# Optimization experiments

Measured on AMD Instinct MI355X. Metric: run time of the kernel, lower is better.

The kernel has to match this reference:

```python
import jax, jax.numpy as jnp
import numpy as np

CAR_DIM = 8
ESC_MAX_AGENT = 32
HID = 256
ACTION_DIM = 30
NUM_STATES = 64
BATCH = 8192
ENC_OUT = 1 + CAR_DIM * ESC_MAX_AGENT          # 257
Q_IN = 1 + CAR_DIM + CAR_DIM * ESC_MAX_AGENT   # 265


def setup_inputs() -> dict:
    key = jax.random.key(0)
    ks = jax.random.split(key, 9)
    s = jax.random.normal(ks[0], (BATCH, CAR_DIM + NUM_STATES * CAR_DIM), dtype=jnp.float32)
    def lin(k, fan_in, fan_out):
        bound = 1.0 / np.sqrt(fan_in)
        kw, kb = jax.random.split(k)
        W = jax.random.uniform(kw, (fan_in, fan_out), jnp.float32, -bound, bound)
        b = jax.random.uniform(kb, (fan_out,), jnp.float32, -bound, bound)
        return W, b
    W1, b1 = lin(ks[1], CAR_DIM, HID)
    W2, b2 = lin(ks[2], HID, ENC_OUT)
    Qw1, Qb1 = lin(ks[3], Q_IN, HID)
    Qw2, Qb2 = lin(ks[4], HID, ACTION_DIM)
    return {"s": s, "W1": W1, "b1": b1, "W2": W2, "b2": b2,
            "Qw1": Qw1, "Qb1": Qb1, "Qw2": Qw2, "Qb2": Qb2}


def reference(s, W1, b1, W2, b2, Qw1, Qb1, Qw2, Qb2):
    B = s.shape[0]
    self_states = s[:, :CAR_DIM]                                   # [B, C]
    surr = s[:, CAR_DIM:].reshape(B, -1, CAR_DIM)                  # [B, N, C]
    # sentinel agents: any coordinate exactly == -1 is skipped
    valid = ~jnp.any(surr == -1.0, axis=-1)                        # [B, N] bool
    h = jax.nn.relu(jnp.einsum('bnc,ch->bnh', surr, W1) + b1)      # [B, N, HID]
    enc = jax.nn.relu(jnp.einsum('bnh,he->bne', h, W2) + b2)       # [B, N, ENC_OUT]
    sum_outputs = jnp.sum(enc * valid[:, :, None].astype(enc.dtype), axis=1)  # [B, ENC_OUT]
    x = jnp.concatenate([self_states, sum_outputs], axis=1)        # [B, Q_IN]
    q = jax.nn.relu(x @ Qw1 + Qb1) @ Qw2 + Qb2                     # [B, ACTION_DIM]
    return q
```

## Files before the change

kernel.cpp:

```cpp
#include <hip/hip_runtime.h>

#define CAR 8
#define SROW 520
#define HID 256
#define EOUT 257
#define XPAD 288
#define ADIM 30

typedef __attribute__((ext_vector_type(8))) short sh8;
typedef __attribute__((ext_vector_type(4))) float f32x4;

__device__ __forceinline__ short f2bf(float f) {
  unsigned u = __builtin_bit_cast(unsigned, f);
  u += 0x7fffu + ((u >> 16) & 1u);
  return (short)(u >> 16);
}
__device__ __forceinline__ unsigned f2bf2(float a, float b) {
  unsigned ua = __builtin_bit_cast(unsigned, a);
  ua += 0x7fffu + ((ua >> 16) & 1u);
  unsigned ub = __builtin_bit_cast(unsigned, b);
  ub += 0x7fffu + ((ub >> 16) & 1u);
  return __builtin_amdgcn_perm(ub, ua, 0x07060302);
}
__device__ __forceinline__ unsigned pkt(float a, float b) {
  return __builtin_amdgcn_perm(__builtin_bit_cast(unsigned, b),
                               __builtin_bit_cast(unsigned, a), 0x07060302);
}

__global__ void k_prep(const float* __restrict__ W1, const float* __restrict__ b1,
                       const float* __restrict__ W2,
                       const float* __restrict__ Qw1, const float* __restrict__ Qw2,
                       short* __restrict__ w1f, short* __restrict__ w2f,
                       short* __restrict__ w3f, short* __restrict__ wq2f) {
  int idx = blockIdx.x * 256 + threadIdx.x;
  if (idx < 8192) {
    int mt = idx >> 9, r = idx & 511, lane = r >> 3, j = r & 7;
    int quad = lane >> 4, m = lane & 15;
    int hid = mt * 16 + m;
    float v = (quad == 0) ? W1[j * HID + hid]
            : (quad == 1 && j == 0) ? b1[hid] : 0.0f;
    w1f[idx] = f2bf(v);
    return;
  }
  int i2 = idx - 8192;
  if (i2 < 69632) {
    int ks = i2 / 8704, r = i2 % 8704;
    int nt = r >> 9, r2 = r & 511, lane = r2 >> 3, j = r2 & 7;
    int quad = lane >> 4, m = lane & 15;
    int k = ks * 32 + quad * 8 + j, n = nt * 16 + m;
    float v = (n < EOUT) ? W2[k * EOUT + n] : 0.0f;
    w2f[i2] = f2bf(v);
    return;
  }
  int i3 = i2 - 69632;
  if (i3 < 73728) {
    int ks = i3 >> 13, r = i3 & 8191;
    int nt = r >> 9, r2 = r & 511, lane = r2 >> 3, j = r2 & 7;
    int quad = lane >> 4, m = lane & 15;
    int k = ks * 32 + quad * 8 + j, n = nt * 16 + m;
    float v = (k < 265) ? Qw1[k * HID + n] : 0.0f;
    w3f[i3] = f2bf(v);
    return;
  }
  int i4 = i3 - 73728;
  if (i4 < 8192) {
    int ks = i4 >> 10, r = i4 & 1023;
    int nt = r >> 9, r2 = r & 511, lane = r2 >> 3, j = r2 & 7;
    int quad = lane >> 4, m = lane & 15;
    int k = ks * 32 + quad * 8 + j, n = nt * 16 + m;
    float v = (n < ADIM) ? Qw2[k * ADIM + n] : 0.0f;
    wq2f[i4] = f2bf(v);
  }
}

__global__ __launch_bounds__(256, 2)
void k_enc(const float* __restrict__ s, const short* __restrict__ w1f,
           const short* __restrict__ w2f, const float* __restrict__ b2,
           float* __restrict__ so288, int B) {
  __shared__ __align__(16) short hlds[2][16384];
  __shared__ float ninvp[4];

  const int tid = threadIdx.x;
  const int w = tid >> 6, lane = tid & 63;
  const int q = lane >> 4, m = lane & 15;
  const int be = w >> 1, half = w & 1;
  const size_t b0 = 2 * (size_t)blockIdx.x;
  int bg = (int)b0 + be; if (bg >= B) bg = B - 1;

  const float* srow0 = s + (size_t)bg * SROW + CAR;
  int4 pk = {0, 0, 0, 0};
  bool inv = false;
  if (lane < 32) {
    const float* sr = srow0 + (half * 32 + lane) * CAR;
    float4 f0 = ((const float4*)sr)[0], f1 = ((const float4*)sr)[1];
    inv = (f0.x == -1.f) | (f0.y == -1.f) | (f0.z == -1.f) | (f0.w == -1.f) |
          (f1.x == -1.f) | (f1.y == -1.f) | (f1.z == -1.f) | (f1.w == -1.f);
    if (!inv) {
      pk.x = (int)f2bf2(f0.x, f0.y); pk.y = (int)f2bf2(f0.z, f0.w);
      pk.z = (int)f2bf2(f1.x, f1.y); pk.w = (int)f2bf2(f1.z, f1.w);
    }
  }
  const float vflag = inv ? 0.f : 1.f;
  unsigned long long bal = __ballot(inv);
  if (lane == 0) ninvp[w] = (float)__popcll(bal);

  int4 p0, p1;
  p0.x = __shfl(pk.x, m, 64);      p0.y = __shfl(pk.y, m, 64);
  p0.z = __shfl(pk.z, m, 64);      p0.w = __shfl(pk.w, m, 64);
  p1.x = __shfl(pk.x, 16 + m, 64); p1.y = __shfl(pk.y, 16 + m, 64);
  p1.z = __shfl(pk.z, 16 + m, 64); p1.w = __shfl(pk.w, 16 + m, 64);
  const float vv0 = __shfl(vflag, m, 64);
  const float vv1 = __shfl(vflag, 16 + m, 64);
  if (q == 1) {
    p0.x = (vv0 != 0.f) ? 0x3f80 : 0; p0.y = p0.z = p0.w = 0;
    p1.x = (vv1 != 0.f) ? 0x3f80 : 0; p1.y = p1.z = p1.w = 0;
  } else if (q >= 2) {
    p0.x = p0.y = p0.z = p0.w = 0;   p1.x = p1.y = p1.z = p1.w = 0;
  }
  sh8 bs0 = __builtin_bit_cast(sh8, p0);
  sh8 bs1 = __builtin_bit_cast(sh8, p1);

  const int T0 = half * 2, T1 = half * 2 + 1;
#pragma unroll
  for (int mt = 0; mt < 16; ++mt) {
    sh8 af = *(const sh8*)(w1f + (mt * 64 + lane) * 8);
    f32x4 z = {0.f, 0.f, 0.f, 0.f};
    f32x4 c0 = __builtin_amdgcn_mfma_f32_16x16x32_bf16(af, bs0, z, 0, 0, 0);
    f32x4 c1 = __builtin_amdgcn_mfma_f32_16x16x32_bf16(af, bs1, z, 0, 0, 0);
    const int hidb = mt * 16 + q * 4;
    const int ks = hidb >> 5, qB = (hidb >> 3) & 3, js = hidb & 7;
    uint2 k0, k1;
    k0.x = pkt(fmaxf(c0[0], 0.f), fmaxf(c0[1], 0.f));
    k0.y = pkt(fmaxf(c0[2], 0.f), fmaxf(c0[3], 0.f));
    k1.x = pkt(fmaxf(c1[0], 0.f), fmaxf(c1[1], 0.f));
    k1.y = pkt(fmaxf(c1[2], 0.f), fmaxf(c1[3], 0.f));
    *(uint2*)(&hlds[be][((T0 * 8 + ks) * 64 + qB * 16 + m) * 8 + js]) = k0;
    *(uint2*)(&hlds[be][((T1 * 8 + ks) * 64 + qB * 16 + m) * 8 + js]) = k1;
  }
  __syncthreads();

  f32x4 acc[4][5][2];
#pragma unroll
  for (int mt = 0; mt < 4; ++mt)
#pragma unroll
    for (int i = 0; i < 5; ++i)
#pragma unroll
      for (int e = 0; e < 2; ++e) {
        f32x4 z = {0.f, 0.f, 0.f, 0.f};
        acc[mt][i][e] = z;
      }

  if (w == 0) {
    sh8 Bf[5];
#pragma unroll
    for (int i = 0; i < 5; ++i) {
      const int t = (i < 4) ? i : 16;
      Bf[i] = *(const sh8*)(w2f + ((0 * 17 + t) * 64 + lane) * 8);
    }
#pragma unroll
    for (int ks = 0; ks < 8; ++ks) {
      sh8 Bn[5];
      if (ks < 7) {
#pragma unroll
        for (int i = 0; i < 5; ++i) {
          const int t = (i < 4) ? i : 16;
          Bn[i] = *(const sh8*)(w2f + (((ks + 1) * 17 + t) * 64 + lane) * 8);
        }
      }
#pragma unroll
      for (int e = 0; e < 2; ++e) {
        sh8 A[4];
#pragma unroll
        for (int mt = 0; mt < 4; ++mt)
          A[mt] = *(const sh8*)(&hlds[e][((mt * 8 + ks) * 64 + lane) * 8]);
#pragma unroll
        for (int i = 0; i < 5; ++i)
#pragma unroll
          for (int mt = 0; mt < 4; ++mt)
            acc[mt][i][e] = __builtin_amdgcn_mfma_f32_16x16x32_bf16(A[mt], Bf[i], acc[mt][i][e], 0, 0, 0);
      }
      if (ks < 7) {
#pragma unroll
        for (int i = 0; i < 5; ++i) Bf[i] = Bn[i];
      }
    }
  } else {
    const int t0 = 4 * w;
    sh8 Bf[4];
#pragma unroll
    for (int i = 0; i < 4; ++i)
      Bf[i] = *(const sh8*)(w2f + ((0 * 17 + t0 + i) * 64 + lane) * 8);
#pragma unroll
    for (int ks = 0; ks < 8; ++ks) {
      sh8 Bn[4];
      if (ks < 7) {
#pragma unroll
        for (int i = 0; i < 4; ++i)
          Bn[i] = *(const sh8*)(w2f + (((ks + 1) * 17 + t0 + i) * 64 + lane) * 8);
      }
#pragma unroll
      for (int e = 0; e < 2; ++e) {
        sh8 A[4];
#pragma unroll
        for (int mt = 0; mt < 4; ++mt)
          A[mt] = *(const sh8*)(&hlds[e][((mt * 8 + ks) * 64 + lane) * 8]);
#pragma unroll
        for (int i = 0; i < 4; ++i)
#pragma unroll
          for (int mt = 0; mt < 4; ++mt)
            acc[mt][i][e] = __builtin_amdgcn_mfma_f32_16x16x32_bf16(A[mt], Bf[i], acc[mt][i][e], 0, 0, 0);
      }
      if (ks < 7) {
#pragma unroll
        for (int i = 0; i < 4; ++i) Bf[i] = Bn[i];
      }
    }
  }

  const float ninv[2] = {ninvp[0] + ninvp[1], ninvp[2] + ninvp[3]};
#pragma unroll
  for (int i = 0; i < 5; ++i) {
    if (i == 4 && w != 0) continue;
    const int t = (i < 4) ? 4 * w + i : 16;
    const int col = t * 16 + m;
    const float b2c = (col < EOUT) ? b2[col] : 0.f;
    const float rb2 = fmaxf(b2c, 0.f);
#pragma unroll
    for (int e = 0; e < 2; ++e) {
      float ssum = 0.f;
#pragma unroll
      for (int mt = 0; mt < 4; ++mt)
#pragma unroll
        for (int r = 0; r < 4; ++r)
          ssum += fmaxf(acc[mt][i][e][r] + b2c, 0.f);
      ssum += __shfl_xor(ssum, 16, 64);
      ssum += __shfl_xor(ssum, 32, 64);
      ssum -= ninv[e] * rb2;
      if (q == 0)
        so288[(b0 + e) * XPAD + CAR + col] = ssum;
    }
  }
  if (w == 1 || w == 2) {
    size_t rr = b0 + (w - 1); if (rr >= (size_t)B) rr = B - 1;
    if (lane < CAR)       so288[rr * XPAD + lane] = s[rr * SROW + lane];
    else if (lane < 16)   so288[rr * XPAD + 280 + (lane - 8)] = 0.f;
  }
}

__global__ __launch_bounds__(256, 2)
void k_q(const float* __restrict__ so288, const short* __restrict__ w3f,
         const float* __restrict__ Qb1, const short* __restrict__ wq2f,
         const float* __restrict__ Qb2, float* __restrict__ out, int B) {
  __shared__ __align__(16) short xf[2 * 9 * 64 * 8];
  __shared__ __align__(16) float H[32 * 260];
  const int tid = threadIdx.x;
  const int w = tid >> 6, lane = tid & 63;
  const int q = lane >> 4, m = lane & 15;
  const int b0 = blockIdx.x * 32;

#pragma unroll
  for (int it = 0; it < 5; ++it) {
    int sidx = tid + it * 256;
    if (sidx < 1152) {
      int mt = sidx / 576, rem = sidx % 576;
      int ks = rem >> 6, l = rem & 63;
      int lq = l >> 4, lm = l & 15;
      int row = b0 + mt * 16 + lm; if (row >= B) row = B - 1;
      const float* xp = so288 + (size_t)row * XPAD + ks * 32 + lq * 8;
      float4 xa = ((const float4*)xp)[0], xb = ((const float4*)xp)[1];
      int4 t = {(int)f2bf2(xa.x, xa.y), (int)f2bf2(xa.z, xa.w),
                (int)f2bf2(xb.x, xb.y), (int)f2bf2(xb.z, xb.w)};
      *(int4*)(xf + sidx * 8) = t;
    }
  }
  __syncthreads();

  f32x4 acc1[2][4];
#pragma unroll
  for (int mt = 0; mt < 2; ++mt)
#pragma unroll
    for (int i = 0; i < 4; ++i) {
      f32x4 z = {0.f, 0.f, 0.f, 0.f};
      acc1[mt][i] = z;
    }
#pragma unroll
  for (int ks = 0; ks < 9; ++ks) {
    sh8 A0 = *(const sh8*)(xf + ((0 * 9 + ks) * 64 + lane) * 8);
    sh8 A1 = *(const sh8*)(xf + ((1 * 9 + ks) * 64 + lane) * 8);
#pragma unroll
    for (int i = 0; i < 4; ++i) {
      sh8 Bf = *(const sh8*)(w3f + ((ks * 16 + 4 * w + i) * 64 + lane) * 8);
      acc1[0][i] = __builtin_amdgcn_mfma_f32_16x16x32_bf16(A0, Bf, acc1[0][i], 0, 0, 0);
      acc1[1][i] = __builtin_amdgcn_mfma_f32_16x16x32_bf16(A1, Bf, acc1[1][i], 0, 0, 0);
    }
  }
#pragma unroll
  for (int i = 0; i < 4; ++i) {
    const int hcol = (4 * w + i) * 16 + m;
    const float bq = Qb1[hcol];
#pragma unroll
    for (int mt = 0; mt < 2; ++mt)
#pragma unroll
      for (int r = 0; r < 4; ++r)
        H[(mt * 16 + q * 4 + r) * 260 + hcol] = fmaxf(acc1[mt][i][r] + bq, 0.f);
  }
  __syncthreads();

  const int mt2 = w >> 1, nt2 = w & 1;
  f32x4 acc2 = {0.f, 0.f, 0.f, 0.f};
#pragma unroll
  for (int ks = 0; ks < 8; ++ks) {
    const float* hp = H + (mt2 * 16 + m) * 260 + ks * 32 + q * 8;
    float4 ha = ((const float4*)hp)[0], hb = ((const float4*)hp)[1];
    int4 t = {(int)f2bf2(ha.x, ha.y), (int)f2bf2(ha.z, ha.w),
              (int)f2bf2(hb.x, hb.y), (int)f2bf2(hb.z, hb.w)};
    sh8 A2 = __builtin_bit_cast(sh8, t);
    sh8 Bf = *(const sh8*)(wq2f + ((ks * 2 + nt2) * 64 + lane) * 8);
    acc2 = __builtin_amdgcn_mfma_f32_16x16x32_bf16(A2, Bf, acc2, 0, 0, 0);
  }
  const int act = nt2 * 16 + m;
  if (act < ADIM) {
    const float bq = Qb2[act];
#pragma unroll
    for (int r = 0; r < 4; ++r) {
      const int row = b0 + mt2 * 16 + q * 4 + r;
      if (row < B) out[(size_t)row * ADIM + act] = acc2[r] + bq;
    }
  }
}

extern "C" void kernel_launch(void* const* d_in, const int* in_sizes, int n_in,
                              void* d_out, int out_size, void* d_ws, size_t ws_size,
                              hipStream_t stream) {
  const float* s   = (const float*)d_in[0];
  const float* W1  = (const float*)d_in[1];
  const float* b1  = (const float*)d_in[2];
  const float* W2  = (const float*)d_in[3];
  const float* b2  = (const float*)d_in[4];
  const float* Qw1 = (const float*)d_in[5];
  const float* Qb1 = (const float*)d_in[6];
  const float* Qw2 = (const float*)d_in[7];
  const float* Qb2 = (const float*)d_in[8];
  float* out = (float*)d_out;
  const int B = in_sizes[0] / SROW;

  char* wsb = (char*)d_ws;
  float* so288 = (float*)wsb;
  size_t off = (size_t)B * XPAD * sizeof(float);
  short* w1f  = (short*)(wsb + off);            off += 8192 * 2;
  short* w2f  = (short*)(wsb + off);            off += 69632 * 2;
  short* w3f  = (short*)(wsb + off);            off += 73728 * 2;
  short* wq2f = (short*)(wsb + off);

  const int prep_elems = 8192 + 69632 + 73728 + 8192;
  k_prep<<<(prep_elems + 255) / 256, 256, 0, stream>>>(W1, b1, W2, Qw1, Qw2,
                                                       w1f, w2f, w3f, wq2f);
  k_enc<<<(B + 1) / 2, 256, 0, stream>>>(s, w1f, w2f, b2, so288, B);
  k_q<<<(B + 31) / 32, 256, 0, stream>>>(so288, w3f, Qb1, wq2f, Qb2, out, B);
}
```

Baseline: 160.3 us.

## Process one batch row per encoder block to cut registers and raise occupancy

The encoder kernel now handles one batch element per block instead of two. Each wave computes 16 agents in the first layer, and the 257th output column tile is split across all four waves, with the partial sums reduced through a small shared buffer. Accumulator registers and shared memory per block are halved and launch bounds go to 4 blocks per CU, aiming at higher occupancy and better latency hiding. The cost is twice as many blocks, each W2 fragment being loaded from global memory once per batch row instead of once per two rows, and an extra barrier per block.

```diff
diff --git a/kernel.cpp b/kernel.cpp
--- a/kernel.cpp
+++ b/kernel.cpp
@@ -73,25 +73,24 @@
   }
 }
 
-__global__ __launch_bounds__(256, 2)
+__global__ __launch_bounds__(256, 4)
 void k_enc(const float* __restrict__ s, const short* __restrict__ w1f,
            const short* __restrict__ w2f, const float* __restrict__ b2,
            float* __restrict__ so288, int B) {
-  __shared__ __align__(16) short hlds[2][16384];
+  __shared__ __align__(16) short hlds[16384];
   __shared__ float ninvp[4];
+  __shared__ float t16[4][16];
 
   const int tid = threadIdx.x;
   const int w = tid >> 6, lane = tid & 63;
   const int q = lane >> 4, m = lane & 15;
-  const int be = w >> 1, half = w & 1;
-  const size_t b0 = 2 * (size_t)blockIdx.x;
-  int bg = (int)b0 + be; if (bg >= B) bg = B - 1;
-
-  const float* srow0 = s + (size_t)bg * SROW + CAR;
+  const size_t bg = blockIdx.x;
+
+  const float* srow0 = s + bg * SROW + CAR;
   int4 pk = {0, 0, 0, 0};
   bool inv = false;
-  if (lane < 32) {
-    const float* sr = srow0 + (half * 32 + lane) * CAR;
+  if (lane < 16) {
+    const float* sr = srow0 + (w * 16 + lane) * CAR;
     float4 f0 = ((const float4*)sr)[0], f1 = ((const float4*)sr)[1];
     inv = (f0.x == -1.f) | (f0.y == -1.f) | (f0.z == -1.f) | (f0.w == -1.f) |
           (f1.x == -1.f) | (f1.y == -1.f) | (f1.z == -1.f) | (f1.w == -1.f);
@@ -104,146 +103,99 @@
   unsigned long long bal = __ballot(inv);
   if (lane == 0) ninvp[w] = (float)__popcll(bal);
 
-  int4 p0, p1;
-  p0.x = __shfl(pk.x, m, 64);      p0.y = __shfl(pk.y, m, 64);
-  p0.z = __shfl(pk.z, m, 64);      p0.w = __shfl(pk.w, m, 64);
-  p1.x = __shfl(pk.x, 16 + m, 64); p1.y = __shfl(pk.y, 16 + m, 64);
-  p1.z = __shfl(pk.z, 16 + m, 64); p1.w = __shfl(pk.w, 16 + m, 64);
+  if (w == 1) {
+    if (lane < CAR)       so288[bg * XPAD + lane] = s[bg * SROW + lane];
+    else if (lane < 16)   so288[bg * XPAD + 280 + (lane - 8)] = 0.f;
+  }
+
+  int4 p0;
+  p0.x = __shfl(pk.x, m, 64); p0.y = __shfl(pk.y, m, 64);
+  p0.z = __shfl(pk.z, m, 64); p0.w = __shfl(pk.w, m, 64);
   const float vv0 = __shfl(vflag, m, 64);
-  const float vv1 = __shfl(vflag, 16 + m, 64);
   if (q == 1) {
     p0.x = (vv0 != 0.f) ? 0x3f80 : 0; p0.y = p0.z = p0.w = 0;
-    p1.x = (vv1 != 0.f) ? 0x3f80 : 0; p1.y = p1.z = p1.w = 0;
   } else if (q >= 2) {
-    p0.x = p0.y = p0.z = p0.w = 0;   p1.x = p1.y = p1.z = p1.w = 0;
-  }
-  sh8 bs0 = __builtin_bit_cast(sh8, p0);
-  sh8 bs1 = __builtin_bit_cast(sh8, p1);
-
-  const int T0 = half * 2, T1 = half * 2 + 1;
-#pragma unroll
+    p0.x = p0.y = p0.z = p0.w = 0;
+  }
+  sh8 bs = __builtin_bit_cast(sh8, p0);
+
+#pragma unroll 4
   for (int mt = 0; mt < 16; ++mt) {
     sh8 af = *(const sh8*)(w1f + (mt * 64 + lane) * 8);
     f32x4 z = {0.f, 0.f, 0.f, 0.f};
-    f32x4 c0 = __builtin_amdgcn_mfma_f32_16x16x32_bf16(af, bs0, z, 0, 0, 0);
-    f32x4 c1 = __builtin_amdgcn_mfma_f32_16x16x32_bf16(af, bs1, z, 0, 0, 0);
+    f32x4 c0 = __builtin_amdgcn_mfma_f32_16x16x32_bf16(af, bs, z, 0, 0, 0);
     const int hidb = mt * 16 + q * 4;
     const int ks = hidb >> 5, qB = (hidb >> 3) & 3, js = hidb & 7;
-    uint2 k0, k1;
+    uint2 k0;
     k0.x = pkt(fmaxf(c0[0], 0.f), fmaxf(c0[1], 0.f));
     k0.y = pkt(fmaxf(c0[2], 0.f), fmaxf(c0[3], 0.f));
-    k1.x = pkt(fmaxf(c1[0], 0.f), fmaxf(c1[1], 0.f));
-    k1.y = pkt(fmaxf(c1[2], 0.f), fmaxf(c1[3], 0.f));
-    *(uint2*)(&hlds[be][((T0 * 8 + ks) * 64 + qB * 16 + m) * 8 + js]) = k0;
-    *(uint2*)(&hlds[be][((T1 * 8 + ks) * 64 + qB * 16 + m) * 8 + js]) = k1;
+    *(uint2*)(&hlds[((w * 8 + ks) * 64 + qB * 16 + m) * 8 + js]) = k0;
   }
   __syncthreads();
 
-  f32x4 acc[4][5][2];
-#pragma unroll
-  for (int mt = 0; mt < 4; ++mt)
-#pragma unroll
-    for (int i = 0; i < 5; ++i)
-#pragma unroll
-      for (int e = 0; e < 2; ++e) {
-        f32x4 z = {0.f, 0.f, 0.f, 0.f};
-        acc[mt][i][e] = z;
-      }
-
-  if (w == 0) {
-    sh8 Bf[5];
-#pragma unroll
-    for (int i = 0; i < 5; ++i) {
-      const int t = (i < 4) ? i : 16;
-      Bf[i] = *(const sh8*)(w2f + ((0 * 17 + t) * 64 + lane) * 8);
-    }
-#pragma unroll
-    for (int ks = 0; ks < 8; ++ks) {
-      sh8 Bn[5];
-      if (ks < 7) {
-#pragma unroll
-        for (int i = 0; i < 5; ++i) {
-          const int t = (i < 4) ? i : 16;
-          Bn[i] = *(const sh8*)(w2f + (((ks + 1) * 17 + t) * 64 + lane) * 8);
-        }
-      }
-#pragma unroll
-      for (int e = 0; e < 2; ++e) {
-        sh8 A[4];
-#pragma unroll
-        for (int mt = 0; mt < 4; ++mt)
-          A[mt] = *(const sh8*)(&hlds[e][((mt * 8 + ks) * 64 + lane) * 8]);
-#pragma unroll
-        for (int i = 0; i < 5; ++i)
-#pragma unroll
-          for (int mt = 0; mt < 4; ++mt)
-            acc[mt][i][e] = __builtin_amdgcn_mfma_f32_16x16x32_bf16(A[mt], Bf[i], acc[mt][i][e], 0, 0, 0);
-      }
-      if (ks < 7) {
-#pragma unroll
-        for (int i = 0; i < 5; ++i) Bf[i] = Bn[i];
-      }
-    }
-  } else {
-    const int t0 = 4 * w;
-    sh8 Bf[4];
-#pragma unroll
-    for (int i = 0; i < 4; ++i)
-      Bf[i] = *(const sh8*)(w2f + ((0 * 17 + t0 + i) * 64 + lane) * 8);
-#pragma unroll
-    for (int ks = 0; ks < 8; ++ks) {
-      sh8 Bn[4];
-      if (ks < 7) {
-#pragma unroll
-        for (int i = 0; i < 4; ++i)
-          Bn[i] = *(const sh8*)(w2f + (((ks + 1) * 17 + t0 + i) * 64 + lane) * 8);
-      }
-#pragma unroll
-      for (int e = 0; e < 2; ++e) {
-        sh8 A[4];
-#pragma unroll
-        for (int mt = 0; mt < 4; ++mt)
-          A[mt] = *(const sh8*)(&hlds[e][((mt * 8 + ks) * 64 + lane) * 8]);
-#pragma unroll
-        for (int i = 0; i < 4; ++i)
-#pragma unroll
-          for (int mt = 0; mt < 4; ++mt)
-            acc[mt][i][e] = __builtin_amdgcn_mfma_f32_16x16x32_bf16(A[mt], Bf[i], acc[mt][i][e], 0, 0, 0);
-      }
-      if (ks < 7) {
-#pragma unroll
-        for (int i = 0; i < 4; ++i) Bf[i] = Bn[i];
-      }
-    }
-  }
-
-  const float ninv[2] = {ninvp[0] + ninvp[1], ninvp[2] + ninvp[3]};
-#pragma unroll
-  for (int i = 0; i < 5; ++i) {
-    if (i == 4 && w != 0) continue;
-    const int t = (i < 4) ? 4 * w + i : 16;
-    const int col = t * 16 + m;
-    const float b2c = (col < EOUT) ? b2[col] : 0.f;
-    const float rb2 = fmaxf(b2c, 0.f);
-#pragma unroll
-    for (int e = 0; e < 2; ++e) {
-      float ssum = 0.f;
-#pragma unroll
-      for (int mt = 0; mt < 4; ++mt)
-#pragma unroll
-        for (int r = 0; r < 4; ++r)
-          ssum += fmaxf(acc[mt][i][e][r] + b2c, 0.f);
-      ssum += __shfl_xor(ssum, 16, 64);
-      ssum += __shfl_xor(ssum, 32, 64);
-      ssum -= ninv[e] * rb2;
-      if (q == 0)
-        so288[(b0 + e) * XPAD + CAR + col] = ssum;
-    }
-  }
-  if (w == 1 || w == 2) {
-    size_t rr = b0 + (w - 1); if (rr >= (size_t)B) rr = B - 1;
-    if (lane < CAR)       so288[rr * XPAD + lane] = s[rr * SROW + lane];
-    else if (lane < 16)   so288[rr * XPAD + 280 + (lane - 8)] = 0.f;
+  f32x4 acc[4][4];
+  f32x4 acc16 = {0.f, 0.f, 0.f, 0.f};
+#pragma unroll
+  for (int mtA = 0; mtA < 4; ++mtA)
+#pragma unroll
+    for (int i = 0; i < 4; ++i) {
+      f32x4 z = {0.f, 0.f, 0.f, 0.f};
+      acc[mtA][i] = z;
+    }
+  const int t0 = 4 * w;
+#pragma unroll 2
+  for (int ks = 0; ks < 8; ++ks) {
+    sh8 A0 = *(const sh8*)(&hlds[((0 * 8 + ks) * 64 + lane) * 8]);
+    sh8 A1 = *(const sh8*)(&hlds[((1 * 8 + ks) * 64 + lane) * 8]);
+    sh8 A2 = *(const sh8*)(&hlds[((2 * 8 + ks) * 64 + lane) * 8]);
+    sh8 A3 = *(const sh8*)(&hlds[((3 * 8 + ks) * 64 + lane) * 8]);
+    sh8 A16 = *(const sh8*)(&hlds[((w * 8 + ks) * 64 + lane) * 8]);
+#pragma unroll
+    for (int i = 0; i < 4; ++i) {
+      sh8 Bf = *(const sh8*)(w2f + ((ks * 17 + t0 + i) * 64 + lane) * 8);
+      acc[0][i] = __builtin_amdgcn_mfma_f32_16x16x32_bf16(A0, Bf, acc[0][i], 0, 0, 0);
+      acc[1][i] = __builtin_amdgcn_mfma_f32_16x16x32_bf16(A1, Bf, acc[1][i], 0, 0, 0);
+      acc[2][i] = __builtin_amdgcn_mfma_f32_16x16x32_bf16(A2, Bf, acc[2][i], 0, 0, 0);
+      acc[3][i] = __builtin_amdgcn_mfma_f32_16x16x32_bf16(A3, Bf, acc[3][i], 0, 0, 0);
+    }
+    sh8 B16 = *(const sh8*)(w2f + ((ks * 17 + 16) * 64 + lane) * 8);
+    acc16 = __builtin_amdgcn_mfma_f32_16x16x32_bf16(A16, B16, acc16, 0, 0, 0);
+  }
+
+  const float ninv = ninvp[0] + ninvp[1] + ninvp[2] + ninvp[3];
+#pragma unroll
+  for (int i = 0; i < 4; ++i) {
+    const int col = (t0 + i) * 16 + m;
+    const float b2c = b2[col];
+    float ssum = 0.f;
+#pragma unroll
+    for (int mtA = 0; mtA < 4; ++mtA)
+#pragma unroll
+      for (int r = 0; r < 4; ++r)
+        ssum += fmaxf(acc[mtA][i][r] + b2c, 0.f);
+    ssum += __shfl_xor(ssum, 16, 64);
+    ssum += __shfl_xor(ssum, 32, 64);
+    ssum -= ninv * fmaxf(b2c, 0.f);
+    if (q == 0) so288[bg * XPAD + CAR + col] = ssum;
+  }
+  {
+    const int colc = 256 + m;
+    const float b2c = (colc < EOUT) ? b2[colc] : 0.f;
+    float s16 = 0.f;
+#pragma unroll
+    for (int r = 0; r < 4; ++r)
+      s16 += fmaxf(acc16[r] + b2c, 0.f);
+    s16 += __shfl_xor(s16, 16, 64);
+    s16 += __shfl_xor(s16, 32, 64);
+    if (q == 0) t16[w][m] = s16;
+  }
+  __syncthreads();
+  if (w == 0 && q == 0) {
+    const int colc = 256 + m;
+    const float b2c = (colc < EOUT) ? b2[colc] : 0.f;
+    const float tot = t16[0][m] + t16[1][m] + t16[2][m] + t16[3][m]
+                    - ninv * fmaxf(b2c, 0.f);
+    so288[bg * XPAD + CAR + colc] = tot;
   }
 }
 
@@ -355,6 +307,6 @@
   const int prep_elems = 8192 + 69632 + 73728 + 8192;
   k_prep<<<(prep_elems + 255) / 256, 256, 0, stream>>>(W1, b1, W2, Qw1, Qw2,
                                                        w1f, w2f, w3f, wq2f);
-  k_enc<<<(B + 1) / 2, 256, 0, stream>>>(s, w1f, w2f, b2, so288, B);
+  k_enc<<<B, 256, 0, stream>>>(s, w1f, w2f, b2, so288, B);
   k_q<<<(B + 31) / 32, 256, 0, stream>>>(so288, w3f, Qb1, wq2f, Qb2, out, B);
 }
```

New measurement: 173.9 us. 1.09x slower.
